# Performance work log

Measured on AMD Instinct MI355X. Metric: run time of the kernel, lower is better.

The kernel has to match this reference:

```python
import jax, jax.numpy as jnp
import numpy as np
from jax import lax

HEIGHT, WIDTH = 13, 10
HIDDEN = 256
CONV_OUT = 32 * 3 * 2  # 192, matches torch _get_conv_output_size


def setup_inputs() -> dict:
    key = jax.random.key(0)
    ks = jax.random.split(key, 12)
    B, T = 128, 512
    s = 0.05
    return {
        "x": jax.random.normal(ks[0], (B, T, HEIGHT, WIDTH), jnp.float32),
        "conv1_w": jax.random.normal(ks[1], (16, 1, 3, 3), jnp.float32) * s,
        "conv1_b": jax.random.normal(ks[2], (16,), jnp.float32) * s,
        "conv2_w": jax.random.normal(ks[3], (32, 16, 3, 3), jnp.float32) * s,
        "conv2_b": jax.random.normal(ks[4], (32,), jnp.float32) * s,
        "W_ih": jax.random.normal(ks[5], (4 * HIDDEN, CONV_OUT), jnp.float32) * s,
        "b_ih": jax.random.normal(ks[6], (4 * HIDDEN,), jnp.float32) * s,
        "W_hh": jax.random.normal(ks[7], (4 * HIDDEN, HIDDEN), jnp.float32) * s,
        "b_hh": jax.random.normal(ks[8], (4 * HIDDEN,), jnp.float32) * s,
        "cls_w": jax.random.normal(ks[9], (64, HIDDEN), jnp.float32) * s,
        "cls_b": jax.random.normal(ks[10], (64,), jnp.float32) * s,
    }


def _conv2d(x, w, b):
    # NCHW, OIHW, padding=1 (SAME for 3x3)
    y = lax.conv_general_dilated(x, w, window_strides=(1, 1),
                                 padding=((1, 1), (1, 1)),
                                 dimension_numbers=("NCHW", "OIHW", "NCHW"))
    return y + b[None, :, None, None]


def _maxpool2(x):
    # kernel 2, stride 2, VALID (floor) like nn.MaxPool2d(2)
    return lax.reduce_window(x, -jnp.inf, lax.max,
                             (1, 1, 2, 2), (1, 1, 2, 2), "VALID")


def reference(x, conv1_w, conv1_b, conv2_w, conv2_b, W_ih, b_ih, W_hh, b_hh, cls_w, cls_b):
    B, T, Hd, Wd = x.shape
    xi = x.reshape(B * T, 1, Hd, Wd)
    y = _maxpool2(jax.nn.relu(_conv2d(xi, conv1_w, conv1_b)))
    y = _maxpool2(jax.nn.relu(_conv2d(y, conv2_w, conv2_b)))
    feat = y.reshape(B, T, -1)  # [B, T, 192], channel-major flatten matches torch view

    # Precompute input contribution to gates for all steps (same math, batched)
    gx_all = jnp.einsum("btf,gf->btg", feat, W_ih) + b_ih + b_hh  # [B, T, 4H]
    H = W_hh.shape[1]

    def step(carry, gx):
        h, c = carry
        gates = gx + h @ W_hh.T  # [B, 4H]
        i, f, g, o = jnp.split(gates, 4, axis=1)
        i = jax.nn.sigmoid(i)
        f = jax.nn.sigmoid(f)
        g = jnp.tanh(g)
        o = jax.nn.sigmoid(o)
        c = f * c + i * g
        h = o * jnp.tanh(c)
        return (h, c), None

    h0 = jnp.zeros((B, H), x.dtype)
    c0 = jnp.zeros((B, H), x.dtype)
    (hT, _), _ = lax.scan(step, (h0, c0), jnp.swapaxes(gx_all, 0, 1))
    logits = hT @ cls_w.T + cls_b
    return logits
```

## Files before the change

kernel.cpp:

```cpp
#include <hip/hip_runtime.h>
#include <hip/hip_bf16.h>


typedef _Float16 half2v __attribute__((ext_vector_type(2)));
typedef _Float16 f16x8 __attribute__((ext_vector_type(8)));
typedef float f32x4 __attribute__((ext_vector_type(4)));

__device__ __forceinline__ float dot2f16(half2v a, half2v b, float c) {
#if defined(__has_builtin)
#if __has_builtin(__builtin_amdgcn_fdot2)
    return __builtin_amdgcn_fdot2(a, b, c, false);
#else
    return c + (float)a.x * (float)b.x + (float)a.y * (float)b.y;
#endif
#else
    return c + (float)a.x * (float)b.x + (float)a.y * (float)b.y;
#endif
}

__device__ __forceinline__ float dot2u(unsigned int a, unsigned int b, float c) {
    return dot2f16(__builtin_bit_cast(half2v, a), __builtin_bit_cast(half2v, b), c);
}

__device__ __forceinline__ unsigned int packf2(const float* p) {
    half2v hv;
    hv.x = (_Float16)p[0];
    hv.y = (_Float16)p[1];
    return __builtin_bit_cast(unsigned int, hv);
}

__device__ __forceinline__ unsigned int packff(float a, float b) {
    half2v hv;
    hv.x = (_Float16)a;
    hv.y = (_Float16)b;
    return __builtin_bit_cast(unsigned int, hv);
}

__device__ __forceinline__ half2v bch2(unsigned int u) {
    return __builtin_bit_cast(half2v, u);
}

__device__ __forceinline__ uint4 pack8(const float* p) {
    uint4 v;
    v.x = packf2(p + 0);
    v.y = packf2(p + 2);
    v.z = packf2(p + 4);
    v.w = packf2(p + 6);
    return v;
}

__global__ __launch_bounds__(256) void prepack_w_kernel(
    const float* __restrict__ Wih, uint4* __restrict__ wf)
{
    int idx = blockIdx.x * 256 + threadIdx.x;
    if (idx < 1024 * 192 / 8) wf[idx] = pack8(Wih + idx * 8);
}

__global__ __launch_bounds__(256) void prepack_sw_kernel(
    const float* __restrict__ Whh, uint4* __restrict__ sw)
{
    int idx = blockIdx.x * 256 + threadIdx.x;
    if (idx < 12 * 1024) {
        int c = idx >> 10, r = idx & 1023;
        sw[idx] = pack8(Whh + (size_t)r * 256 + 160 + 8 * c);
    }
}

__global__ __launch_bounds__(256) void conv_kernel(
    const float* __restrict__ x,
    const float* __restrict__ c1w,
    const float* __restrict__ c1b,
    const float* __restrict__ c2w,
    const float* __restrict__ c2b,
    _Float16* __restrict__ feat)
{
    __shared__ float w1t[9 * 16];
    __shared__ float b1s[16];
    __shared__ unsigned int w2h[8 * 9 * 32];
    __shared__ float b2s[32];
    __shared__ float xp[4][14 * 12];
    __shared__ __align__(4) _Float16 p1ph[4][8 * 7 * 16];

    const int tid = threadIdx.x;

    for (int idx = tid; idx < 144; idx += 256) {
        int oc = idx / 9, k = idx % 9;
        w1t[k * 16 + oc] = c1w[idx];
    }
    if (tid < 16) b1s[tid] = c1b[tid];
    for (int idx = tid; idx < 2304; idx += 256) {
        int icp = idx / 288, rem = idx % 288;
        int k = rem / 32, oc = rem % 32;
        float a = c2w[oc * 144 + (2 * icp) * 9 + k];
        float b = c2w[oc * 144 + (2 * icp + 1) * 9 + k];
        w2h[idx] = packff(a, b);
    }
    if (tid < 32) b2s[tid] = c2b[tid];

    const int w = tid >> 6;
    const int lane = tid & 63;
    const int img = blockIdx.x * 4 + w;

    for (int i = lane; i < 14 * 12; i += 64) xp[w][i] = 0.f;
    for (int i = lane; i < 8 * 7 * 16; i += 64) p1ph[w][i] = (_Float16)0.f;
    __syncthreads();

    const float* xin = x + (size_t)img * 130;
    for (int i = lane; i < 130; i += 64) {
        int r = i / 10, c = i % 10;
        xp[w][(r + 1) * 12 + (c + 1)] = xin[i];
    }
    __syncthreads();

    {
        const int oc = lane & 15, q = lane >> 4;
        #pragma unroll
        for (int i = 0; i < 8; i++) {
            int pos = i * 4 + q;
            if (pos < 30) {
                int ph = pos / 5, pw = pos % 5;
                float cmax = -1e30f;
                #pragma unroll
                for (int pt = 0; pt < 4; pt++) {
                    int Y = 2 * ph + (pt >> 1), X = 2 * pw + (pt & 1);
                    float s = 0.f;
                    #pragma unroll
                    for (int k = 0; k < 9; k++) {
                        int dy = k / 3, dx = k % 3;
                        s += w1t[k * 16 + oc] * xp[w][(Y + dy) * 12 + X + dx];
                    }
                    cmax = fmaxf(cmax, s);
                }
                p1ph[w][((ph + 1) * 7 + (pw + 1)) * 16 + oc] =
                    (_Float16)fmaxf(0.f, cmax + b1s[oc]);
            }
        }
    }
    __syncthreads();

    {
        const int oc = lane & 31, pw2 = lane >> 5;
        float acc[3][4] = {};
        const _Float16* P = &p1ph[w][0];

        #pragma unroll
        for (int icp = 0; icp < 8; icp++) {
            unsigned int hreg[32];
            #pragma unroll
            for (int y = 0; y < 8; y++)
                #pragma unroll
                for (int xx = 0; xx < 4; xx++) {
                    int xcol = 2 * pw2 + xx;
                    hreg[y * 4 + xx] =
                        *(const unsigned int*)&P[(y * 7 + xcol) * 16 + 2 * icp];
                }
            #pragma unroll
            for (int k = 0; k < 9; k++) {
                int dy = k / 3, dx = k % 3;
                unsigned int wv = w2h[(icp * 9 + k) * 32 + oc];
                #pragma unroll
                for (int ph2 = 0; ph2 < 3; ph2++) {
                    #pragma unroll
                    for (int pt = 0; pt < 4; pt++) {
                        int y = 2 * ph2 + (pt >> 1) + dy;
                        int xx2 = (pt & 1) + dx;
                        acc[ph2][pt] = dot2u(wv, hreg[y * 4 + xx2], acc[ph2][pt]);
                    }
                }
            }
        }
        float bias = b2s[oc];
        _Float16* fo = feat + (size_t)img * 192;
        #pragma unroll
        for (int ph2 = 0; ph2 < 3; ph2++) {
            float m = fmaxf(fmaxf(acc[ph2][0], acc[ph2][1]),
                            fmaxf(acc[ph2][2], acc[ph2][3]));
            fo[oc * 6 + ph2 * 2 + pw2] = (_Float16)fmaxf(0.f, m + bias);
        }
    }
}

__global__ __launch_bounds__(256) void gemm_gx_kernel(
    const _Float16* __restrict__ feat,
    const _Float16* __restrict__ wf16,
    const float* __restrict__ bih,
    const float* __restrict__ bhh,
    _Float16* __restrict__ gx)
{
    __shared__ uint4 As4[128][13];
    __shared__ uint4 Ws4[128][13];

    const int tid = threadIdx.x;
    const int n0 = blockIdx.x * 128;
    const int m0 = blockIdx.y * 128;

    const int w = tid >> 6;
    const int lane = tid & 63;
    const int lm = lane & 15;
    const int lk = lane >> 4;

    f32x4 acc[2][8] = {};

    #pragma unroll
    for (int half = 0; half < 2; half++) {
        if (half) __syncthreads();
        const int kbase = half * 12;
        #pragma unroll
        for (int it = 0; it < 6; it++) {
            int q = tid + it * 256;
            int r = q / 12, c = q % 12;
            As4[r][c] = *(const uint4*)(feat + (size_t)(m0 + r) * 192 + (kbase + c) * 8);
            Ws4[r][c] = *(const uint4*)(wf16 + (size_t)(n0 + r) * 192 + (kbase + c) * 8);
        }
        __syncthreads();

        #pragma unroll
        for (int ks = 0; ks < 3; ks++) {
            f16x8 wf[2], af[8];
            #pragma unroll
            for (int nf = 0; nf < 2; nf++)
                wf[nf] = __builtin_bit_cast(f16x8, Ws4[w * 32 + nf * 16 + lm][ks * 4 + lk]);
            #pragma unroll
            for (int mf = 0; mf < 8; mf++)
                af[mf] = __builtin_bit_cast(f16x8, As4[mf * 16 + lm][ks * 4 + lk]);
            #pragma unroll
            for (int nf = 0; nf < 2; nf++)
                #pragma unroll
                for (int mf = 0; mf < 8; mf++)
                    acc[nf][mf] = __builtin_amdgcn_mfma_f32_16x16x32_f16(
                        wf[nf], af[mf], acc[nf][mf], 0, 0, 0);
        }
    }

    #pragma unroll
    for (int nf = 0; nf < 2; nf++) {
        int nb = n0 + w * 32 + nf * 16 + lk * 4;
        float4 b1 = *(const float4*)&bih[nb];
        float4 b2 = *(const float4*)&bhh[nb];
        float bs0 = b1.x + b2.x, bs1 = b1.y + b2.y;
        float bs2 = b1.z + b2.z, bs3 = b1.w + b2.w;
        #pragma unroll
        for (int mf = 0; mf < 8; mf++) {
            int m = m0 + mf * 16 + lm;
            union { _Float16 h[4]; uint2 u; } pk;
            pk.h[0] = (_Float16)(acc[nf][mf][0] + bs0);
            pk.h[1] = (_Float16)(acc[nf][mf][1] + bs1);
            pk.h[2] = (_Float16)(acc[nf][mf][2] + bs2);
            pk.h[3] = (_Float16)(acc[nf][mf][3] + bs3);
            *(uint2*)&gx[(size_t)m * 1024 + nb] = pk.u;
        }
    }
}

__global__ __launch_bounds__(512, 2) void lstm_kernel(
    const _Float16* __restrict__ gx,
    const float* __restrict__ Whh,
    const uint4* __restrict__ sw,
    const float* __restrict__ clsw,
    const float* __restrict__ clsb,
    float* __restrict__ out)
{
    __shared__ uint4 wl4[9][1024];
    __shared__ uint2 wl2[1024];
    __shared__ __align__(16) _Float16 hbuf[2][256];
    __shared__ float xg[512];

    const int t = threadIdx.x;
    const int b = blockIdx.x;
    const int r0 = t, r1 = t + 512;

    const float* w0 = Whh + (size_t)r0 * 256;
    const float* w1 = Whh + (size_t)r1 * 256;

    #pragma unroll
    for (int ch = 0; ch < 9; ch++) {
        wl4[ch][r0] = pack8(w0 + 8 * ch);
        wl4[ch][r1] = pack8(w1 + 8 * ch);
    }
    {
        uint2 v0, v1;
        v0.x = packf2(w0 + 72); v0.y = packf2(w0 + 74);
        v1.x = packf2(w1 + 72); v1.y = packf2(w1 + 74);
        wl2[r0] = v0;
        wl2[r1] = v1;
    }
    half2v wr0[42], wr1[42];
    #pragma unroll
    for (int q = 0; q < 42; q++) {
        wr0[q] = bch2(packf2(w0 + 76 + 2 * q));
        wr1[q] = bch2(packf2(w1 + 76 + 2 * q));
    }
    if (t < 256) hbuf[0][t] = (_Float16)0.f;
    __syncthreads();

    float c = 0.f;
    int cur = 0;
    const _Float16* gxb = gx + (size_t)b * 512 * 1024;
    float ga = (float)gxb[r0];
    float gb = (float)gxb[r1];

    for (int step = 0; step < 512; step++) {
        const _Float16* gxn = gxb + (size_t)((step + 1) & 511) * 1024;
        _Float16 na = gxn[r0];
        _Float16 nb = gxn[r1];

        float acc0 = ga, acc1 = gb;
        const uint4* hb4 = (const uint4*)&hbuf[cur][0];

        #pragma unroll
        for (int sc = 0; sc < 12; sc++) {
            uint4 u0 = sw[sc * 1024 + r0];
            uint4 u1 = sw[sc * 1024 + r1];
            uint4 hv = hb4[20 + sc];
            acc0 = dot2f16(bch2(u0.x), bch2(hv.x), acc0);
            acc0 = dot2f16(bch2(u0.y), bch2(hv.y), acc0);
            acc0 = dot2f16(bch2(u0.z), bch2(hv.z), acc0);
            acc0 = dot2f16(bch2(u0.w), bch2(hv.w), acc0);
            acc1 = dot2f16(bch2(u1.x), bch2(hv.x), acc1);
            acc1 = dot2f16(bch2(u1.y), bch2(hv.y), acc1);
            acc1 = dot2f16(bch2(u1.z), bch2(hv.z), acc1);
            acc1 = dot2f16(bch2(u1.w), bch2(hv.w), acc1);
        }
        #pragma unroll
        for (int ch = 0; ch < 9; ch++) {
            uint4 u0 = wl4[ch][r0];
            uint4 u1 = wl4[ch][r1];
            uint4 hv = hb4[ch];
            acc0 = dot2f16(bch2(u0.x), bch2(hv.x), acc0);
            acc0 = dot2f16(bch2(u0.y), bch2(hv.y), acc0);
            acc0 = dot2f16(bch2(u0.z), bch2(hv.z), acc0);
            acc0 = dot2f16(bch2(u0.w), bch2(hv.w), acc0);
            acc1 = dot2f16(bch2(u1.x), bch2(hv.x), acc1);
            acc1 = dot2f16(bch2(u1.y), bch2(hv.y), acc1);
            acc1 = dot2f16(bch2(u1.z), bch2(hv.z), acc1);
            acc1 = dot2f16(bch2(u1.w), bch2(hv.w), acc1);
        }
        {
            uint4 hv = hb4[9];
            uint2 u0 = wl2[r0];
            uint2 u1 = wl2[r1];
            acc0 = dot2f16(bch2(u0.x), bch2(hv.x), acc0);
            acc0 = dot2f16(bch2(u0.y), bch2(hv.y), acc0);
            acc1 = dot2f16(bch2(u1.x), bch2(hv.x), acc1);
            acc1 = dot2f16(bch2(u1.y), bch2(hv.y), acc1);
            acc0 = dot2f16(wr0[0], bch2(hv.z), acc0);
            acc0 = dot2f16(wr0[1], bch2(hv.w), acc0);
            acc1 = dot2f16(wr1[0], bch2(hv.z), acc1);
            acc1 = dot2f16(wr1[1], bch2(hv.w), acc1);
        }
        #pragma unroll
        for (int cc = 0; cc < 10; cc++) {
            uint4 hv = hb4[10 + cc];
            acc0 = dot2f16(wr0[2 + 4 * cc + 0], bch2(hv.x), acc0);
            acc0 = dot2f16(wr0[2 + 4 * cc + 1], bch2(hv.y), acc0);
            acc0 = dot2f16(wr0[2 + 4 * cc + 2], bch2(hv.z), acc0);
            acc0 = dot2f16(wr0[2 + 4 * cc + 3], bch2(hv.w), acc0);
            acc1 = dot2f16(wr1[2 + 4 * cc + 0], bch2(hv.x), acc1);
            acc1 = dot2f16(wr1[2 + 4 * cc + 1], bch2(hv.y), acc1);
            acc1 = dot2f16(wr1[2 + 4 * cc + 2], bch2(hv.z), acc1);
            acc1 = dot2f16(wr1[2 + 4 * cc + 3], bch2(hv.w), acc1);
        }

        if (t >= 256) {
            xg[t - 256] = acc0;
            xg[t] = acc1;
        }
        __syncthreads();
        if (t < 256) {
            float i_ = 1.f / (1.f + __expf(-acc0));
            float g_ = 1.f - 2.f / (__expf(2.f * acc1) + 1.f);
            float f_ = 1.f / (1.f + __expf(-xg[t]));
            float o_ = 1.f / (1.f + __expf(-xg[t + 256]));
            c = f_ * c + i_ * g_;
            float th = 1.f - 2.f / (__expf(2.f * c) + 1.f);
            float h = o_ * th;
            hbuf[cur ^ 1][t] = (_Float16)h;
        }
        __syncthreads();
        cur ^= 1;
        ga = (float)na;
        gb = (float)nb;
    }

    if (t < 64) {
        const float* cw = clsw + t * 256;
        float s = clsb[t];
        for (int k = 0; k < 256; k++) s += cw[k] * (float)hbuf[cur][k];
        out[b * 64 + t] = s;
    }
}

extern "C" void kernel_launch(void* const* d_in, const int* in_sizes, int n_in,
                              void* d_out, int out_size, void* d_ws, size_t ws_size,
                              hipStream_t stream) {
    const float* x    = (const float*)d_in[0];
    const float* c1w  = (const float*)d_in[1];
    const float* c1b  = (const float*)d_in[2];
    const float* c2w  = (const float*)d_in[3];
    const float* c2b  = (const float*)d_in[4];
    const float* Wih  = (const float*)d_in[5];
    const float* bih  = (const float*)d_in[6];
    const float* Whh  = (const float*)d_in[7];
    const float* bhh  = (const float*)d_in[8];
    const float* clsw = (const float*)d_in[9];
    const float* clsb = (const float*)d_in[10];

    _Float16* feat = (_Float16*)d_ws;
    _Float16* gx   = feat + (size_t)65536 * 192;
    uint4* aux     = (uint4*)(gx + (size_t)65536 * 1024);
    float* outp = (float*)d_out;

    hipLaunchKernelGGL(prepack_w_kernel, dim3(96), dim3(256), 0, stream, Wih, aux);
    hipLaunchKernelGGL(conv_kernel, dim3(16384), dim3(256), 0, stream,
                       x, c1w, c1b, c2w, c2b, feat);
    hipLaunchKernelGGL(gemm_gx_kernel, dim3(8, 512), dim3(256), 0, stream,
                       feat, (const _Float16*)aux, bih, bhh, gx);
    hipLaunchKernelGGL(prepack_sw_kernel, dim3(48), dim3(256), 0, stream, Whh, aux);
    hipLaunchKernelGGL(lstm_kernel, dim3(128), dim3(512), 0, stream,
                       gx, Whh, aux, clsw, clsb, outp);
}
```

Measured before the change: 1.106 ms.

## Give each LSTM thread all four gates of one hidden unit

The LSTM kernel now runs 256 threads per block. Each thread computes all four gate rows (i, f, g, o) for one hidden unit, so the gate exchange through shared memory and its extra barrier per step are gone. The register-resident slice of W_hh grows to 4x49 half2 per thread, the global-streamed part shrinks from 12 to 10 chunks, and a new one-word LDS array covers the remainder. The cost is fewer waves per block to hide latency and very high register pressure, with possible spills.

```diff
diff --git a/kernel.cpp b/kernel.cpp
--- a/kernel.cpp
+++ b/kernel.cpp
@@ -60,9 +60,9 @@
     const float* __restrict__ Whh, uint4* __restrict__ sw)
 {
     int idx = blockIdx.x * 256 + threadIdx.x;
-    if (idx < 12 * 1024) {
+    if (idx < 10 * 1024) {
         int c = idx >> 10, r = idx & 1023;
-        sw[idx] = pack8(Whh + (size_t)r * 256 + 160 + 8 * c);
+        sw[idx] = pack8(Whh + (size_t)r * 256 + 176 + 8 * c);
     }
 }
 
@@ -252,7 +252,7 @@
     }
 }
 
-__global__ __launch_bounds__(512, 2) void lstm_kernel(
+__global__ __launch_bounds__(256, 1) void lstm_kernel(
     const _Float16* __restrict__ gx,
     const float* __restrict__ Whh,
     const uint4* __restrict__ sw,
@@ -262,124 +262,130 @@
 {
     __shared__ uint4 wl4[9][1024];
     __shared__ uint2 wl2[1024];
+    __shared__ unsigned int wl1[1024];
     __shared__ __align__(16) _Float16 hbuf[2][256];
-    __shared__ float xg[512];
 
     const int t = threadIdx.x;
     const int b = blockIdx.x;
-    const int r0 = t, r1 = t + 512;
-
-    const float* w0 = Whh + (size_t)r0 * 256;
-    const float* w1 = Whh + (size_t)r1 * 256;
-
+
+    half2v wr[4][49];
     #pragma unroll
-    for (int ch = 0; ch < 9; ch++) {
-        wl4[ch][r0] = pack8(w0 + 8 * ch);
-        wl4[ch][r1] = pack8(w1 + 8 * ch);
-    }
-    {
-        uint2 v0, v1;
-        v0.x = packf2(w0 + 72); v0.y = packf2(w0 + 74);
-        v1.x = packf2(w1 + 72); v1.y = packf2(w1 + 74);
-        wl2[r0] = v0;
-        wl2[r1] = v1;
-    }
-    half2v wr0[42], wr1[42];
-    #pragma unroll
-    for (int q = 0; q < 42; q++) {
-        wr0[q] = bch2(packf2(w0 + 76 + 2 * q));
-        wr1[q] = bch2(packf2(w1 + 76 + 2 * q));
-    }
-    if (t < 256) hbuf[0][t] = (_Float16)0.f;
+    for (int g = 0; g < 4; g++) {
+        const int row = t + 256 * g;
+        const float* wp = Whh + (size_t)row * 256;
+        #pragma unroll
+        for (int ch = 0; ch < 9; ch++) wl4[ch][row] = pack8(wp + 8 * ch);
+        uint2 v2;
+        v2.x = packf2(wp + 72);
+        v2.y = packf2(wp + 74);
+        wl2[row] = v2;
+        wl1[row] = packf2(wp + 76);
+        #pragma unroll
+        for (int q = 0; q < 49; q++) wr[g][q] = bch2(packf2(wp + 78 + 2 * q));
+    }
+    hbuf[0][t] = (_Float16)0.f;
     __syncthreads();
 
     float c = 0.f;
     int cur = 0;
     const _Float16* gxb = gx + (size_t)b * 512 * 1024;
-    float ga = (float)gxb[r0];
-    float gb = (float)gxb[r1];
+    float ga0 = (float)gxb[t];
+    float ga1 = (float)gxb[t + 256];
+    float ga2 = (float)gxb[t + 512];
+    float ga3 = (float)gxb[t + 768];
 
     for (int step = 0; step < 512; step++) {
         const _Float16* gxn = gxb + (size_t)((step + 1) & 511) * 1024;
-        _Float16 na = gxn[r0];
-        _Float16 nb = gxn[r1];
-
-        float acc0 = ga, acc1 = gb;
+        _Float16 n0 = gxn[t];
+        _Float16 n1 = gxn[t + 256];
+        _Float16 n2 = gxn[t + 512];
+        _Float16 n3 = gxn[t + 768];
+
+        float a0 = ga0, a1 = ga1, a2 = ga2, a3 = ga3;
         const uint4* hb4 = (const uint4*)&hbuf[cur][0];
 
         #pragma unroll
-        for (int sc = 0; sc < 12; sc++) {
-            uint4 u0 = sw[sc * 1024 + r0];
-            uint4 u1 = sw[sc * 1024 + r1];
-            uint4 hv = hb4[20 + sc];
-            acc0 = dot2f16(bch2(u0.x), bch2(hv.x), acc0);
-            acc0 = dot2f16(bch2(u0.y), bch2(hv.y), acc0);
-            acc0 = dot2f16(bch2(u0.z), bch2(hv.z), acc0);
-            acc0 = dot2f16(bch2(u0.w), bch2(hv.w), acc0);
-            acc1 = dot2f16(bch2(u1.x), bch2(hv.x), acc1);
-            acc1 = dot2f16(bch2(u1.y), bch2(hv.y), acc1);
-            acc1 = dot2f16(bch2(u1.z), bch2(hv.z), acc1);
-            acc1 = dot2f16(bch2(u1.w), bch2(hv.w), acc1);
+        for (int sc = 0; sc < 10; sc++) {
+            uint4 u0 = sw[sc * 1024 + t];
+            uint4 u1 = sw[sc * 1024 + t + 256];
+            uint4 u2 = sw[sc * 1024 + t + 512];
+            uint4 u3 = sw[sc * 1024 + t + 768];
+            uint4 hv = hb4[22 + sc];
+            a0 = dot2u(u0.x, hv.x, a0); a0 = dot2u(u0.y, hv.y, a0);
+            a0 = dot2u(u0.z, hv.z, a0); a0 = dot2u(u0.w, hv.w, a0);
+            a1 = dot2u(u1.x, hv.x, a1); a1 = dot2u(u1.y, hv.y, a1);
+            a1 = dot2u(u1.z, hv.z, a1); a1 = dot2u(u1.w, hv.w, a1);
+            a2 = dot2u(u2.x, hv.x, a2); a2 = dot2u(u2.y, hv.y, a2);
+            a2 = dot2u(u2.z, hv.z, a2); a2 = dot2u(u2.w, hv.w, a2);
+            a3 = dot2u(u3.x, hv.x, a3); a3 = dot2u(u3.y, hv.y, a3);
+            a3 = dot2u(u3.z, hv.z, a3); a3 = dot2u(u3.w, hv.w, a3);
         }
         #pragma unroll
         for (int ch = 0; ch < 9; ch++) {
-            uint4 u0 = wl4[ch][r0];
-            uint4 u1 = wl4[ch][r1];
+            uint4 u0 = wl4[ch][t];
+            uint4 u1 = wl4[ch][t + 256];
+            uint4 u2 = wl4[ch][t + 512];
+            uint4 u3 = wl4[ch][t + 768];
             uint4 hv = hb4[ch];
-            acc0 = dot2f16(bch2(u0.x), bch2(hv.x), acc0);
-            acc0 = dot2f16(bch2(u0.y), bch2(hv.y), acc0);
-            acc0 = dot2f16(bch2(u0.z), bch2(hv.z), acc0);
-            acc0 = dot2f16(bch2(u0.w), bch2(hv.w), acc0);
-            acc1 = dot2f16(bch2(u1.x), bch2(hv.x), acc1);
-            acc1 = dot2f16(bch2(u1.y), bch2(hv.y), acc1);
-            acc1 = dot2f16(bch2(u1.z), bch2(hv.z), acc1);
-            acc1 = dot2f16(bch2(u1.w), bch2(hv.w), acc1);
+            a0 = dot2u(u0.x, hv.x, a0); a0 = dot2u(u0.y, hv.y, a0);
+            a0 = dot2u(u0.z, hv.z, a0); a0 = dot2u(u0.w, hv.w, a0);
+            a1 = dot2u(u1.x, hv.x, a1); a1 = dot2u(u1.y, hv.y, a1);
+            a1 = dot2u(u1.z, hv.z, a1); a1 = dot2u(u1.w, hv.w, a1);
+            a2 = dot2u(u2.x, hv.x, a2); a2 = dot2u(u2.y, hv.y, a2);
+            a2 = dot2u(u2.z, hv.z, a2); a2 = dot2u(u2.w, hv.w, a2);
+            a3 = dot2u(u3.x, hv.x, a3); a3 = dot2u(u3.y, hv.y, a3);
+            a3 = dot2u(u3.z, hv.z, a3); a3 = dot2u(u3.w, hv.w, a3);
         }
         {
             uint4 hv = hb4[9];
-            uint2 u0 = wl2[r0];
-            uint2 u1 = wl2[r1];
-            acc0 = dot2f16(bch2(u0.x), bch2(hv.x), acc0);
-            acc0 = dot2f16(bch2(u0.y), bch2(hv.y), acc0);
-            acc1 = dot2f16(bch2(u1.x), bch2(hv.x), acc1);
-            acc1 = dot2f16(bch2(u1.y), bch2(hv.y), acc1);
-            acc0 = dot2f16(wr0[0], bch2(hv.z), acc0);
-            acc0 = dot2f16(wr0[1], bch2(hv.w), acc0);
-            acc1 = dot2f16(wr1[0], bch2(hv.z), acc1);
-            acc1 = dot2f16(wr1[1], bch2(hv.w), acc1);
-        }
-        #pragma unroll
-        for (int cc = 0; cc < 10; cc++) {
-            uint4 hv = hb4[10 + cc];
-            acc0 = dot2f16(wr0[2 + 4 * cc + 0], bch2(hv.x), acc0);
-            acc0 = dot2f16(wr0[2 + 4 * cc + 1], bch2(hv.y), acc0);
-            acc0 = dot2f16(wr0[2 + 4 * cc + 2], bch2(hv.z), acc0);
-            acc0 = dot2f16(wr0[2 + 4 * cc + 3], bch2(hv.w), acc0);
-            acc1 = dot2f16(wr1[2 + 4 * cc + 0], bch2(hv.x), acc1);
-            acc1 = dot2f16(wr1[2 + 4 * cc + 1], bch2(hv.y), acc1);
-            acc1 = dot2f16(wr1[2 + 4 * cc + 2], bch2(hv.z), acc1);
-            acc1 = dot2f16(wr1[2 + 4 * cc + 3], bch2(hv.w), acc1);
-        }
-
-        if (t >= 256) {
-            xg[t - 256] = acc0;
-            xg[t] = acc1;
-        }
-        __syncthreads();
-        if (t < 256) {
-            float i_ = 1.f / (1.f + __expf(-acc0));
-            float g_ = 1.f - 2.f / (__expf(2.f * acc1) + 1.f);
-            float f_ = 1.f / (1.f + __expf(-xg[t]));
-            float o_ = 1.f / (1.f + __expf(-xg[t + 256]));
-            c = f_ * c + i_ * g_;
-            float th = 1.f - 2.f / (__expf(2.f * c) + 1.f);
-            float h = o_ * th;
-            hbuf[cur ^ 1][t] = (_Float16)h;
-        }
+            uint2 u20 = wl2[t];
+            uint2 u21 = wl2[t + 256];
+            uint2 u22 = wl2[t + 512];
+            uint2 u23 = wl2[t + 768];
+            a0 = dot2u(u20.x, hv.x, a0); a0 = dot2u(u20.y, hv.y, a0);
+            a1 = dot2u(u21.x, hv.x, a1); a1 = dot2u(u21.y, hv.y, a1);
+            a2 = dot2u(u22.x, hv.x, a2); a2 = dot2u(u22.y, hv.y, a2);
+            a3 = dot2u(u23.x, hv.x, a3); a3 = dot2u(u23.y, hv.y, a3);
+            a0 = dot2u(wl1[t], hv.z, a0);
+            a1 = dot2u(wl1[t + 256], hv.z, a1);
+            a2 = dot2u(wl1[t + 512], hv.z, a2);
+            a3 = dot2u(wl1[t + 768], hv.z, a3);
+            a0 = dot2f16(wr[0][0], bch2(hv.w), a0);
+            a1 = dot2f16(wr[1][0], bch2(hv.w), a1);
+            a2 = dot2f16(wr[2][0], bch2(hv.w), a2);
+            a3 = dot2f16(wr[3][0], bch2(hv.w), a3);
+        }
+        #pragma unroll
+        for (int j = 0; j < 12; j++) {
+            uint4 hv = hb4[10 + j];
+            a0 = dot2f16(wr[0][1 + 4 * j], bch2(hv.x), a0);
+            a0 = dot2f16(wr[0][2 + 4 * j], bch2(hv.y), a0);
+            a0 = dot2f16(wr[0][3 + 4 * j], bch2(hv.z), a0);
+            a0 = dot2f16(wr[0][4 + 4 * j], bch2(hv.w), a0);
+            a1 = dot2f16(wr[1][1 + 4 * j], bch2(hv.x), a1);
+            a1 = dot2f16(wr[1][2 + 4 * j], bch2(hv.y), a1);
+            a1 = dot2f16(wr[1][3 + 4 * j], bch2(hv.z), a1);
+            a1 = dot2f16(wr[1][4 + 4 * j], bch2(hv.w), a1);
+            a2 = dot2f16(wr[2][1 + 4 * j], bch2(hv.x), a2);
+            a2 = dot2f16(wr[2][2 + 4 * j], bch2(hv.y), a2);
+            a2 = dot2f16(wr[2][3 + 4 * j], bch2(hv.z), a2);
+            a2 = dot2f16(wr[2][4 + 4 * j], bch2(hv.w), a2);
+            a3 = dot2f16(wr[3][1 + 4 * j], bch2(hv.x), a3);
+            a3 = dot2f16(wr[3][2 + 4 * j], bch2(hv.y), a3);
+            a3 = dot2f16(wr[3][3 + 4 * j], bch2(hv.z), a3);
+            a3 = dot2f16(wr[3][4 + 4 * j], bch2(hv.w), a3);
+        }
+
+        float i_ = 1.f / (1.f + __expf(-a0));
+        float f_ = 1.f / (1.f + __expf(-a1));
+        float g_ = 1.f - 2.f / (__expf(2.f * a2) + 1.f);
+        float o_ = 1.f / (1.f + __expf(-a3));
+        c = f_ * c + i_ * g_;
+        float th = 1.f - 2.f / (__expf(2.f * c) + 1.f);
+        hbuf[cur ^ 1][t] = (_Float16)(o_ * th);
         __syncthreads();
         cur ^= 1;
-        ga = (float)na;
-        gb = (float)nb;
+        ga0 = (float)n0; ga1 = (float)n1; ga2 = (float)n2; ga3 = (float)n3;
     }
 
     if (t < 64) {
@@ -415,7 +421,7 @@
                        x, c1w, c1b, c2w, c2b, feat);
     hipLaunchKernelGGL(gemm_gx_kernel, dim3(8, 512), dim3(256), 0, stream,
                        feat, (const _Float16*)aux, bih, bhh, gx);
-    hipLaunchKernelGGL(prepack_sw_kernel, dim3(48), dim3(256), 0, stream, Whh, aux);
-    hipLaunchKernelGGL(lstm_kernel, dim3(128), dim3(512), 0, stream,
+    hipLaunchKernelGGL(prepack_sw_kernel, dim3(40), dim3(256), 0, stream, Whh, aux);
+    hipLaunchKernelGGL(lstm_kernel, dim3(128), dim3(256), 0, stream,
                        gx, Whh, aux, clsw, clsb, outp);
 }
```

New measurement: 1.998 ms. 80.7% more time.
